# Performance work log

Hardware: AMD Instinct MI355X
Metric: run time of the kernel (lower is better)

The kernel has to match this reference:

```python
import jax, jax.numpy as jnp
import numpy as np

B, N, D, H, DK, DV = 2, 2048, 1024, 16, 64, 64
NEG = -1000000000.0
EPS = 1e-6


def setup_inputs() -> dict:
    key = jax.random.key(0)
    ks = jax.random.split(key, 8)
    s = 0.02
    return {
        "q": jax.random.normal(ks[0], (B, N, D), jnp.float32),
        "k": jax.random.normal(ks[1], (B, N, D), jnp.float32),
        "v": jax.random.normal(ks[2], (B, N, D), jnp.float32),
        "attn_mask": jnp.ones((B, N, N), jnp.int32),
        "Wq": jax.random.normal(ks[3], (D, H * DK), jnp.float32) * s,
        "Wk": jax.random.normal(ks[4], (D, H * DK), jnp.float32) * s,
        "Wv": jax.random.normal(ks[5], (D, H * DV), jnp.float32) * s,
        "Wo": jax.random.normal(ks[6], (H * DV, D), jnp.float32) * s,
        "gamma": jnp.ones((D,), jnp.float32),
        "beta": jnp.zeros((D,), jnp.float32),
    }


def reference(q, k, v, attn_mask, Wq, Wk, Wv, Wo, gamma, beta):
    b, n, _ = q.shape
    residual = q
    # project and split heads: (b, h, n, dk)
    qh = (q @ Wq).reshape(b, n, H, DK).transpose(0, 2, 1, 3)
    kh = (k @ Wk).reshape(b, n, H, DK).transpose(0, 2, 1, 3)
    vh = (v @ Wv).reshape(b, n, H, DV).transpose(0, 2, 1, 3)
    temperature = DK ** 0.5
    scores = jnp.einsum('bhnd,bhmd->bhnm', qh / temperature, kh)
    # external mask (masked where mask == 0), broadcast over heads
    scores = jnp.where(attn_mask[:, None, :, :] == 0, NEG, scores)
    # built-in causal mask (strictly upper triangle)
    causal = jnp.triu(jnp.ones((n, n), dtype=bool), k=1)
    scores = jnp.where(causal, NEG, scores)
    attn = jax.nn.softmax(scores, axis=-1)
    out = jnp.einsum('bhnm,bhmd->bnhd', attn, vh).reshape(b, n, H * DV)
    out = out @ Wo + residual
    # LayerNorm(eps=1e-6)
    mean = out.mean(-1, keepdims=True)
    var = ((out - mean) ** 2).mean(-1, keepdims=True)
    out = (out - mean) / jnp.sqrt(var + EPS) * gamma + beta
    return out, attn
```

## Files before the change

### kernel.cpp

```cpp
#include <hip/hip_runtime.h>
#include <hip/hip_bf16.h>
#include <stdint.h>

#define B_ 2
#define N_ 2048
#define D_ 1024
#define H_ 16
#define MM 4096
#define NN 1024
#define KK 1024

typedef __bf16 bf16;
typedef __bf16 bf16x8 __attribute__((ext_vector_type(8)));
typedef float f32x4 __attribute__((ext_vector_type(4)));

struct __align__(8) bf4 { bf16 v[4]; };

#define LDS_STRIDE 144

__global__ void k_wtt(const float* __restrict__ W, bf16* __restrict__ Wt) {
    __shared__ float t[32][33];
    int bx = blockIdx.x * 32, by = blockIdx.y * 32;
    int tx = threadIdx.x, ty = threadIdx.y;
#pragma unroll
    for (int j = 0; j < 32; j += 8)
        t[ty + j][tx] = W[(size_t)(by + ty + j) * 1024 + bx + tx];
    __syncthreads();
#pragma unroll
    for (int j = 0; j < 32; j += 8)
        Wt[(size_t)(bx + ty + j) * 1024 + by + tx] = (bf16)t[tx][ty + j];
}

__global__ __launch_bounds__(256) void k_bits(const int* __restrict__ mask,
                                              uint32_t* __restrict__ bits) {
    size_t flat = (size_t)blockIdx.x * 256 + threadIdx.x;
    int col = (int)(flat & (N_ - 1));
    int row = (int)((flat >> 11) & (N_ - 1));
    bool ok = (mask[flat] != 0) && (col <= row);
    unsigned long long bal = __ballot(ok);
    if ((threadIdx.x & 63) == 0)
        *(unsigned long long*)(bits + (flat >> 5)) = bal;
}

template <int MODE, bool AF32>
__global__ __launch_bounds__(256) void k_gemm(const void* __restrict__ Av,
                                              const bf16* __restrict__ Bt,
                                              bf16* __restrict__ Cb,
                                              float* __restrict__ Cf,
                                              const float* __restrict__ resid,
                                              float scale) {
    __shared__ __align__(16) char AsB[64 * LDS_STRIDE];
    __shared__ __align__(16) char BsB[128 * LDS_STRIDE];
    const int tid = threadIdx.x, lane = tid & 63, w = tid >> 6;
    const int g = lane >> 4, li = lane & 15;
    const int bm0 = blockIdx.x * 64, bn0 = blockIdx.y * 128;
    const int srow = tid >> 3, sc = tid & 7;
    const bf16* Ab = (const bf16*)Av;
    const float* Af = (const float*)Av;

    f32x4 zz = {0.f, 0.f, 0.f, 0.f};
    f32x4 acc[4][2];
#pragma unroll
    for (int mf = 0; mf < 4; ++mf)
#pragma unroll
        for (int nf = 0; nf < 2; ++nf) acc[mf][nf] = zz;

    f32x4 pa0[2], pa1[2];
    bf16x8 pab[2];
    bf16x8 pb[4];

    auto issueA = [&](int k0) {
        if constexpr (AF32) {
#pragma unroll
            for (int i = 0; i < 2; ++i) {
                const float* s = Af + (size_t)(bm0 + srow + 32 * i) * KK + k0 + sc * 8;
                pa0[i] = *(const f32x4*)s;
                pa1[i] = *(const f32x4*)(s + 4);
            }
        } else {
#pragma unroll
            for (int i = 0; i < 2; ++i)
                pab[i] = *(const bf16x8*)(Ab + (size_t)(bm0 + srow + 32 * i) * KK + k0 + sc * 8);
        }
    };
    auto issueB = [&](int k0) {
#pragma unroll
        for (int i = 0; i < 4; ++i)
            pb[i] = *(const bf16x8*)(Bt + (size_t)(bn0 + srow + 32 * i) * KK + k0 + sc * 8);
    };
    auto writeS = [&]() {
#pragma unroll
        for (int i = 0; i < 2; ++i) {
            bf16x8 t;
            if constexpr (AF32) {
#pragma unroll
                for (int j = 0; j < 4; ++j) {
                    t[j] = (bf16)pa0[i][j];
                    t[4 + j] = (bf16)pa1[i][j];
                }
            } else {
                t = pab[i];
            }
            *(bf16x8*)(AsB + (srow + 32 * i) * LDS_STRIDE + sc * 16) = t;
        }
#pragma unroll
        for (int i = 0; i < 4; ++i)
            *(bf16x8*)(BsB + (srow + 32 * i) * LDS_STRIDE + sc * 16) = pb[i];
    };

    issueA(0);
    issueB(0);
    for (int k0 = 0; k0 < KK; k0 += 64) {
        __syncthreads();
        writeS();
        int kn = (k0 + 64 < KK) ? k0 + 64 : k0;
        issueA(kn);
        issueB(kn);
        __syncthreads();
#pragma unroll
        for (int kk = 0; kk < 2; ++kk) {
            const int kb = kk * 64 + (g << 4);
            bf16x8 bfr[2];
#pragma unroll
            for (int nf = 0; nf < 2; ++nf) {
                int rn = w * 32 + nf * 16 + li;
                bfr[nf] = *(const bf16x8*)(BsB + rn * LDS_STRIDE + kb);
            }
#pragma unroll
            for (int mf = 0; mf < 4; ++mf) {
                int rm = mf * 16 + li;
                bf16x8 afr = *(const bf16x8*)(AsB + rm * LDS_STRIDE + kb);
                acc[mf][0] = __builtin_amdgcn_mfma_f32_16x16x32_bf16(
                    afr, bfr[0], acc[mf][0], 0, 0, 0);
                acc[mf][1] = __builtin_amdgcn_mfma_f32_16x16x32_bf16(
                    afr, bfr[1], acc[mf][1], 0, 0, 0);
            }
        }
    }
#pragma unroll
    for (int mf = 0; mf < 4; ++mf)
#pragma unroll
        for (int nf = 0; nf < 2; ++nf) {
            int n = bn0 + w * 32 + nf * 16 + li;
            int m0 = bm0 + mf * 16 + (g << 2);
            if (MODE == 0) {
#pragma unroll
                for (int r = 0; r < 4; ++r)
                    Cb[(size_t)(m0 + r) * NN + n] = (bf16)(acc[mf][nf][r] * scale);
            } else if (MODE == 1) {
                int bq = m0 >> 11, tok = m0 & (N_ - 1);
                int hh = n >> 6, dv = n & 63;
                bf4 val;
#pragma unroll
                for (int r = 0; r < 4; ++r) val.v[r] = (bf16)(acc[mf][nf][r] * scale);
                *(bf4*)(Cb + ((size_t)((bq * H_ + hh) * 64 + dv)) * N_ + tok) = val;
            } else {
#pragma unroll
                for (int r = 0; r < 4; ++r) {
                    size_t ix = (size_t)(m0 + r) * NN + n;
                    Cf[ix] = acc[mf][nf][r] + resid[ix];
                }
            }
        }
}

__global__ __launch_bounds__(256) void k_attn(const bf16* __restrict__ Qh,
                                              const bf16* __restrict__ Kh,
                                              const bf16* __restrict__ Vt,
                                              const uint32_t* __restrict__ bits,
                                              float* __restrict__ attnp,
                                              bf16* __restrict__ Ob) {
    __shared__ __align__(16) char Qs[64 * LDS_STRIDE];
    __shared__ __align__(16) char Ks[64 * LDS_STRIDE];
    __shared__ __align__(16) char Vs[64 * LDS_STRIDE];
    __shared__ __align__(16) char Ps[64 * LDS_STRIDE];
    const int tid = threadIdx.x, lane = tid & 63, w = tid >> 6;
    const int g = lane >> 4, li = lane & 15;
    const int p = blockIdx.x, h = blockIdx.y, b = blockIdx.z;
    const int srow = tid >> 3, sc = tid & 7;
    const int myrow = w * 16 + li;

    const size_t kbase = ((size_t)b * N_) * D_ + h * 64;
    const size_t vbase = ((size_t)(b * H_ + h) * 64) * N_;
    f32x4 zz = {0.f, 0.f, 0.f, 0.f};

    for (int half = 0; half < 2; ++half) {
        const int qt = half ? (31 - p) : p;
        const int i0 = qt << 6;
        const size_t abase = (((size_t)b * H_ + h) * N_ + i0) * (size_t)N_;

        __syncthreads();
        {
            const char* qsrc = (const char*)Qh +
                (kbase + (size_t)(i0 + srow) * D_ + sc * 8) * 2;
            bf16x8 t0 = *(const bf16x8*)qsrc;
            bf16x8 t1 = *(const bf16x8*)(qsrc + (size_t)32 * D_ * 2);
            *(bf16x8*)(Qs + srow * LDS_STRIDE + sc * 16) = t0;
            *(bf16x8*)(Qs + (srow + 32) * LDS_STRIDE + sc * 16) = t1;
        }
        const uint32_t* mrow = bits + (((size_t)b * N_ + i0 + myrow) << 6);

        float m = -1e30f, l = 0.f;
        bf16x8 ka, kb2;
        {
            const char* ks = (const char*)Kh + (kbase + (size_t)srow * D_ + sc * 8) * 2;
            ka = *(const bf16x8*)ks;
            kb2 = *(const bf16x8*)(ks + (size_t)32 * D_ * 2);
        }
        for (int jt = 0; jt <= qt; ++jt) {
            __syncthreads();
            *(bf16x8*)(Ks + srow * LDS_STRIDE + sc * 16) = ka;
            *(bf16x8*)(Ks + (srow + 32) * LDS_STRIDE + sc * 16) = kb2;
            {
                int jn = (jt < qt) ? jt + 1 : qt;
                const char* ks = (const char*)Kh +
                    (kbase + (size_t)(jn * 64 + srow) * D_ + sc * 8) * 2;
                ka = *(const bf16x8*)ks;
                kb2 = *(const bf16x8*)(ks + (size_t)32 * D_ * 2);
            }
            uint2 mw = *(const uint2*)(mrow + (jt << 1));
            __syncthreads();

            f32x4 s[4];
#pragma unroll
            for (int mf = 0; mf < 4; ++mf) s[mf] = zz;
#pragma unroll
            for (int kk = 0; kk < 2; ++kk) {
                const int kb = kk * 64 + (g << 4);
                bf16x8 qf = *(const bf16x8*)(Qs + myrow * LDS_STRIDE + kb);
#pragma unroll
                for (int mf = 0; mf < 4; ++mf) {
                    bf16x8 kf = *(const bf16x8*)(Ks + (mf * 16 + li) * LDS_STRIDE + kb);
                    s[mf] = __builtin_amdgcn_mfma_f32_16x16x32_bf16(kf, qf, s[mf], 0, 0, 0);
                }
            }
            float tmax = m;
#pragma unroll
            for (int mf = 0; mf < 4; ++mf) {
                uint32_t wsel = (mf < 2) ? mw.x : mw.y;
#pragma unroll
                for (int r = 0; r < 4; ++r) {
                    int sh = (mf & 1) * 16 + g * 4 + r;
                    float xv = ((wsel >> sh) & 1) ? s[mf][r] : -1e9f;
                    s[mf][r] = xv;
                    tmax = fmaxf(tmax, xv);
                }
            }
            tmax = fmaxf(tmax, __shfl_xor(tmax, 16));
            tmax = fmaxf(tmax, __shfl_xor(tmax, 32));
            float ps = 0.f;
#pragma unroll
            for (int mf = 0; mf < 4; ++mf)
#pragma unroll
                for (int r = 0; r < 4; ++r) ps += __expf(s[mf][r] - tmax);
            ps += __shfl_xor(ps, 16);
            ps += __shfl_xor(ps, 32);
            l = l * __expf(m - tmax) + ps;
            m = tmax;
        }
        const float linv = 1.0f / l;

        f32x4 oacc[4];
#pragma unroll
        for (int nf = 0; nf < 4; ++nf) oacc[nf] = zz;

        bf16x8 va, vb2;
        {
            const char* ks = (const char*)Kh + (kbase + (size_t)srow * D_ + sc * 8) * 2;
            ka = *(const bf16x8*)ks;
            kb2 = *(const bf16x8*)(ks + (size_t)32 * D_ * 2);
            const char* vs = (const char*)Vt + (vbase + (size_t)srow * N_ + sc * 8) * 2;
            va = *(const bf16x8*)vs;
            vb2 = *(const bf16x8*)(vs + (size_t)32 * N_ * 2);
        }
        for (int jt = 0; jt <= qt; ++jt) {
            __syncthreads();
            *(bf16x8*)(Ks + srow * LDS_STRIDE + sc * 16) = ka;
            *(bf16x8*)(Ks + (srow + 32) * LDS_STRIDE + sc * 16) = kb2;
            *(bf16x8*)(Vs + srow * LDS_STRIDE + sc * 16) = va;
            *(bf16x8*)(Vs + (srow + 32) * LDS_STRIDE + sc * 16) = vb2;
            {
                int jn = (jt < qt) ? jt + 1 : qt;
                const char* ks = (const char*)Kh +
                    (kbase + (size_t)(jn * 64 + srow) * D_ + sc * 8) * 2;
                ka = *(const bf16x8*)ks;
                kb2 = *(const bf16x8*)(ks + (size_t)32 * D_ * 2);
                const char* vs = (const char*)Vt +
                    (vbase + (size_t)srow * N_ + jn * 64 + sc * 8) * 2;
                va = *(const bf16x8*)vs;
                vb2 = *(const bf16x8*)(vs + (size_t)32 * N_ * 2);
            }
            uint2 mw = *(const uint2*)(mrow + (jt << 1));
            __syncthreads();

            f32x4 s[4];
#pragma unroll
            for (int mf = 0; mf < 4; ++mf) s[mf] = zz;
#pragma unroll
            for (int kk = 0; kk < 2; ++kk) {
                const int kb = kk * 64 + (g << 4);
                bf16x8 qf = *(const bf16x8*)(Qs + myrow * LDS_STRIDE + kb);
#pragma unroll
                for (int mf = 0; mf < 4; ++mf) {
                    bf16x8 kf = *(const bf16x8*)(Ks + (mf * 16 + li) * LDS_STRIDE + kb);
                    s[mf] = __builtin_amdgcn_mfma_f32_16x16x32_bf16(kf, qf, s[mf], 0, 0, 0);
                }
            }
#pragma unroll
            for (int mf = 0; mf < 4; ++mf) {
                uint32_t wsel = (mf < 2) ? mw.x : mw.y;
#pragma unroll
                for (int r = 0; r < 4; ++r) {
                    int sh = (mf & 1) * 16 + g * 4 + r;
                    float xv = ((wsel >> sh) & 1) ? s[mf][r] : -1e9f;
                    s[mf][r] = __expf(xv - m) * linv;
                }
                *(f32x4*)(attnp + abase + (size_t)myrow * N_ + (jt << 6) + mf * 16 + g * 4) = s[mf];
                bf4 pk;
#pragma unroll
                for (int r = 0; r < 4; ++r) pk.v[r] = (bf16)s[mf][r];
                *(bf4*)(Ps + myrow * LDS_STRIDE + (mf * 16 + g * 4) * 2) = pk;
            }
#pragma unroll
            for (int kk = 0; kk < 2; ++kk) {
                const int kb = kk * 64 + (g << 4);
                bf16x8 pf = *(const bf16x8*)(Ps + myrow * LDS_STRIDE + kb);
#pragma unroll
                for (int nf = 0; nf < 4; ++nf) {
                    bf16x8 vf = *(const bf16x8*)(Vs + (nf * 16 + li) * LDS_STRIDE + kb);
                    oacc[nf] = __builtin_amdgcn_mfma_f32_16x16x32_bf16(pf, vf, oacc[nf], 0, 0, 0);
                }
            }
        }
#pragma unroll
        for (int nf = 0; nf < 4; ++nf)
#pragma unroll
            for (int r = 0; r < 4; ++r) {
                int gi = i0 + w * 16 + g * 4 + r;
                Ob[((size_t)(b * N_ + gi)) * D_ + h * 64 + nf * 16 + li] = (bf16)oacc[nf][r];
            }
        int zc0 = i0 + 64;
        if (zc0 < N_) {
            int r = tid >> 2, tc = tid & 3;
            f32x4 z = zz;
            for (int c = zc0 + tc * 4; c < N_; c += 16)
                *(f32x4*)(attnp + abase + (size_t)r * N_ + c) = z;
        }
    }
}

__global__ __launch_bounds__(256) void k_ln(float* __restrict__ out,
                                            const float* __restrict__ gamma,
                                            const float* __restrict__ beta) {
    const int row = blockIdx.x, t = threadIdx.x, lane = t & 63, w = t >> 6;
    float* p = out + (size_t)row * D_;
    f32x4 x = *(const f32x4*)(p + t * 4);
    float s = x[0] + x[1] + x[2] + x[3];
    float s2 = x[0] * x[0] + x[1] * x[1] + x[2] * x[2] + x[3] * x[3];
#pragma unroll
    for (int o = 1; o < 64; o <<= 1) {
        s += __shfl_xor(s, o);
        s2 += __shfl_xor(s2, o);
    }
    __shared__ float r1[4], r2[4];
    if (lane == 0) { r1[w] = s; r2[w] = s2; }
    __syncthreads();
    s = r1[0] + r1[1] + r1[2] + r1[3];
    s2 = r2[0] + r2[1] + r2[2] + r2[3];
    float mean = s * (1.f / D_);
    float var = s2 * (1.f / D_) - mean * mean;
    float rstd = rsqrtf(var + 1e-6f);
    f32x4 gv = *(const f32x4*)(gamma + t * 4);
    f32x4 bv = *(const f32x4*)(beta + t * 4);
    f32x4 y;
#pragma unroll
    for (int c = 0; c < 4; ++c) y[c] = (x[c] - mean) * rstd * gv[c] + bv[c];
    *(f32x4*)(p + t * 4) = y;
}

extern "C" void kernel_launch(void* const* d_in, const int* in_sizes, int n_in,
                              void* d_out, int out_size, void* d_ws,
                              size_t ws_size, hipStream_t stream) {
    (void)in_sizes; (void)n_in; (void)out_size; (void)ws_size;
    const float* q = (const float*)d_in[0];
    const float* k = (const float*)d_in[1];
    const float* v = (const float*)d_in[2];
    const int* msk = (const int*)d_in[3];
    const float* Wq = (const float*)d_in[4];
    const float* Wk = (const float*)d_in[5];
    const float* Wv = (const float*)d_in[6];
    const float* Wo = (const float*)d_in[7];
    const float* gamma = (const float*)d_in[8];
    const float* beta = (const float*)d_in[9];

    float* outp = (float*)d_out;
    float* attnp = outp + (size_t)B_ * N_ * D_;

    const size_t U = (size_t)B_ * N_ * D_;
    const size_t W1 = (size_t)D_ * D_;
    bf16* ws = (bf16*)d_ws;
    bf16* WqT = ws;  ws += W1;
    bf16* WkT = ws;  ws += W1;
    bf16* WvT = ws;  ws += W1;
    bf16* WoT = ws;  ws += W1;
    bf16* Qh = ws;   ws += U;
    bf16* Kh = ws;   ws += U;
    bf16* Vt = ws;   ws += U;
    bf16* Ob = ws;   ws += U;
    uint32_t* bits = (uint32_t*)ws;

    dim3 tb(32, 8);
    k_wtt<<<dim3(32, 32), tb, 0, stream>>>(Wq, WqT);
    k_wtt<<<dim3(32, 32), tb, 0, stream>>>(Wk, WkT);
    k_wtt<<<dim3(32, 32), tb, 0, stream>>>(Wv, WvT);
    k_wtt<<<dim3(32, 32), tb, 0, stream>>>(Wo, WoT);
    k_bits<<<(size_t)B_ * N_ * N_ / 256, 256, 0, stream>>>(msk, bits);

    dim3 gg(MM / 64, NN / 128);
    k_gemm<0, true><<<gg, 256, 0, stream>>>(q, WqT, Qh, nullptr, nullptr, 0.125f);
    k_gemm<0, true><<<gg, 256, 0, stream>>>(k, WkT, Kh, nullptr, nullptr, 1.0f);
    k_gemm<1, true><<<gg, 256, 0, stream>>>(v, WvT, Vt, nullptr, nullptr, 1.0f);

    k_attn<<<dim3(16, H_, B_), 256, 0, stream>>>(Qh, Kh, Vt, bits, attnp, Ob);

    k_gemm<2, false><<<gg, 256, 0, stream>>>(Ob, WoT, nullptr, outp, q, 1.0f);

    k_ln<<<B_ * N_, 256, 0, stream>>>(outp, gamma, beta);
}
```

Before: 285.9 us.

## Restructure GEMMs with direct-to-LDS loads, batch QKV projections, double-buffer attention

A new kernel converts q/k/v to bf16 up front, and the three projection GEMMs are merged into one launch. The GEMM core now uses 128x128 tiles with global_load_lds direct copies and a swizzled block order. The attention kernel double-buffers its K/V tiles in LDS so the next tile loads while the current one is computed. Attention-probability stores become nontemporal. These target GEMM memory traffic, launch overhead and attention load latency, at the cost of an extra conversion pass and more LDS use.

New measurement: 300.2 us. +5.0%, slower.

```diff
diff --git a/kernel.cpp b/kernel.cpp
--- a/kernel.cpp
+++ b/kernel.cpp
@@ -17,6 +17,29 @@
 struct __align__(8) bf4 { bf16 v[4]; };
 
 #define LDS_STRIDE 144
+
+#define GLDS(gp, lp)                                                     \
+    __builtin_amdgcn_global_load_lds(                                    \
+        (const __attribute__((address_space(1))) void*)(gp),             \
+        (__attribute__((address_space(3))) void*)(lp), 16, 0, 0)
+
+__global__ __launch_bounds__(256) void k_cvt3(const float* __restrict__ q,
+                                              const float* __restrict__ k,
+                                              const float* __restrict__ v,
+                                              bf16* __restrict__ qb,
+                                              bf16* __restrict__ kb,
+                                              bf16* __restrict__ vb) {
+    const int z = blockIdx.y;
+    const float* s = z == 0 ? q : z == 1 ? k : v;
+    bf16* d = z == 0 ? qb : z == 1 ? kb : vb;
+    size_t i = ((size_t)blockIdx.x * 256 + threadIdx.x) * 8;
+    f32x4 a = *(const f32x4*)(s + i);
+    f32x4 b = *(const f32x4*)(s + i + 4);
+    bf16x8 o;
+#pragma unroll
+    for (int j = 0; j < 4; ++j) { o[j] = (bf16)a[j]; o[4 + j] = (bf16)b[j]; }
+    *(bf16x8*)(d + i) = o;
+}
 
 __global__ void k_wtt(const float* __restrict__ W, bf16* __restrict__ Wt) {
     __shared__ float t[32][33];
@@ -42,124 +65,144 @@
         *(unsigned long long*)(bits + (flat >> 5)) = bal;
 }
 
-template <int MODE, bool AF32>
-__global__ __launch_bounds__(256) void k_gemm(const void* __restrict__ Av,
-                                              const bf16* __restrict__ Bt,
-                                              bf16* __restrict__ Cb,
-                                              float* __restrict__ Cf,
-                                              const float* __restrict__ resid,
-                                              float scale) {
-    __shared__ __align__(16) char AsB[64 * LDS_STRIDE];
-    __shared__ __align__(16) char BsB[128 * LDS_STRIDE];
-    const int tid = threadIdx.x, lane = tid & 63, w = tid >> 6;
+__device__ __forceinline__ void mm_core(const bf16* __restrict__ A,
+                                        const bf16* __restrict__ Bt,
+                                        int bm0, int bn0,
+                                        bf16* As, bf16* Bs,
+                                        f32x4 (&acc)[4][4]) {
+    const int tid = threadIdx.x, w = tid >> 6, lane = tid & 63;
     const int g = lane >> 4, li = lane & 15;
-    const int bm0 = blockIdx.x * 64, bn0 = blockIdx.y * 128;
-    const int srow = tid >> 3, sc = tid & 7;
-    const bf16* Ab = (const bf16*)Av;
-    const float* Af = (const float*)Av;
+    const int wr = w >> 1, wc = w & 1;
+    const int row = tid >> 3, cc = tid & 7;
 
     f32x4 zz = {0.f, 0.f, 0.f, 0.f};
-    f32x4 acc[4][2];
 #pragma unroll
     for (int mf = 0; mf < 4; ++mf)
 #pragma unroll
-        for (int nf = 0; nf < 2; ++nf) acc[mf][nf] = zz;
-
-    f32x4 pa0[2], pa1[2];
-    bf16x8 pab[2];
-    bf16x8 pb[4];
-
-    auto issueA = [&](int k0) {
-        if constexpr (AF32) {
-#pragma unroll
-            for (int i = 0; i < 2; ++i) {
-                const float* s = Af + (size_t)(bm0 + srow + 32 * i) * KK + k0 + sc * 8;
-                pa0[i] = *(const f32x4*)s;
-                pa1[i] = *(const f32x4*)(s + 4);
-            }
-        } else {
-#pragma unroll
-            for (int i = 0; i < 2; ++i)
-                pab[i] = *(const bf16x8*)(Ab + (size_t)(bm0 + srow + 32 * i) * KK + k0 + sc * 8);
+        for (int nf = 0; nf < 4; ++nf) acc[mf][nf] = zz;
+
+    auto stage = [&](int k0) {
+#pragma unroll
+        for (int c = 0; c < 4; ++c) {
+            int ch = c * 256 + tid;
+            int r = ch >> 3, cl = ch & 7;
+            GLDS(A + (size_t)(bm0 + r) * KK + k0 + cl * 8,
+                 As + ((size_t)c * 256 + w * 64) * 8);
+        }
+#pragma unroll
+        for (int c = 0; c < 4; ++c) {
+            int ch = c * 256 + tid;
+            int r = ch >> 3, cl = ch & 7;
+            GLDS(Bt + (size_t)(bn0 + r) * KK + k0 + cl * 8,
+                 Bs + ((size_t)c * 256 + w * 64) * 8);
         }
     };
-    auto issueB = [&](int k0) {
-#pragma unroll
-        for (int i = 0; i < 4; ++i)
-            pb[i] = *(const bf16x8*)(Bt + (size_t)(bn0 + srow + 32 * i) * KK + k0 + sc * 8);
-    };
-    auto writeS = [&]() {
-#pragma unroll
-        for (int i = 0; i < 2; ++i) {
-            bf16x8 t;
-            if constexpr (AF32) {
-#pragma unroll
-                for (int j = 0; j < 4; ++j) {
-                    t[j] = (bf16)pa0[i][j];
-                    t[4 + j] = (bf16)pa1[i][j];
-                }
-            } else {
-                t = pab[i];
-            }
-            *(bf16x8*)(AsB + (srow + 32 * i) * LDS_STRIDE + sc * 16) = t;
-        }
-#pragma unroll
-        for (int i = 0; i < 4; ++i)
-            *(bf16x8*)(BsB + (srow + 32 * i) * LDS_STRIDE + sc * 16) = pb[i];
-    };
-
-    issueA(0);
-    issueB(0);
-    for (int k0 = 0; k0 < KK; k0 += 64) {
+    (void)row; (void)cc;
+
+    stage(0);
+    for (int s = 0; s < KK / 64; ++s) {
         __syncthreads();
-        writeS();
-        int kn = (k0 + 64 < KK) ? k0 + 64 : k0;
-        issueA(kn);
-        issueB(kn);
+#pragma unroll
+        for (int kk = 0; kk < 2; ++kk) {
+            bf16x8 af[4], bfr[4];
+#pragma unroll
+            for (int i = 0; i < 4; ++i) {
+                af[i] = *(const bf16x8*)(As + (wr * 64 + i * 16 + li) * 64 + kk * 32 + g * 8);
+                bfr[i] = *(const bf16x8*)(Bs + (wc * 64 + i * 16 + li) * 64 + kk * 32 + g * 8);
+            }
+#pragma unroll
+            for (int mf = 0; mf < 4; ++mf)
+#pragma unroll
+                for (int nf = 0; nf < 4; ++nf)
+                    acc[mf][nf] = __builtin_amdgcn_mfma_f32_16x16x32_bf16(
+                        af[mf], bfr[nf], acc[mf][nf], 0, 0, 0);
+        }
         __syncthreads();
-#pragma unroll
-        for (int kk = 0; kk < 2; ++kk) {
-            const int kb = kk * 64 + (g << 4);
-            bf16x8 bfr[2];
-#pragma unroll
-            for (int nf = 0; nf < 2; ++nf) {
-                int rn = w * 32 + nf * 16 + li;
-                bfr[nf] = *(const bf16x8*)(BsB + rn * LDS_STRIDE + kb);
-            }
-#pragma unroll
-            for (int mf = 0; mf < 4; ++mf) {
-                int rm = mf * 16 + li;
-                bf16x8 afr = *(const bf16x8*)(AsB + rm * LDS_STRIDE + kb);
-                acc[mf][0] = __builtin_amdgcn_mfma_f32_16x16x32_bf16(
-                    afr, bfr[0], acc[mf][0], 0, 0, 0);
-                acc[mf][1] = __builtin_amdgcn_mfma_f32_16x16x32_bf16(
-                    afr, bfr[1], acc[mf][1], 0, 0, 0);
-            }
-        }
+        if (s + 1 < KK / 64) stage((s + 1) * 64);
     }
-#pragma unroll
-    for (int mf = 0; mf < 4; ++mf)
-#pragma unroll
-        for (int nf = 0; nf < 2; ++nf) {
-            int n = bn0 + w * 32 + nf * 16 + li;
-            int m0 = bm0 + mf * 16 + (g << 2);
-            if (MODE == 0) {
+}
+
+__global__ __launch_bounds__(256) void k_proj(const bf16* __restrict__ qb,
+                                              const bf16* __restrict__ kb,
+                                              const bf16* __restrict__ vb,
+                                              const bf16* __restrict__ WqT,
+                                              const bf16* __restrict__ WkT,
+                                              const bf16* __restrict__ WvT,
+                                              bf16* __restrict__ Qh,
+                                              bf16* __restrict__ Kh,
+                                              bf16* __restrict__ Vt) {
+    __shared__ __align__(16) bf16 As[128 * 64];
+    __shared__ __align__(16) bf16 Bs[128 * 64];
+    const int z = blockIdx.y;
+    const bf16* A = z == 0 ? qb : z == 1 ? kb : vb;
+    const bf16* Bt = z == 0 ? WqT : z == 1 ? WkT : WvT;
+    int bid = blockIdx.x;
+    int swz = (bid & 7) * 32 + (bid >> 3);
+    int bm0 = (swz >> 3) * 128, bn0 = (swz & 7) * 128;
+
+    f32x4 acc[4][4];
+    mm_core(A, Bt, bm0, bn0, As, Bs, acc);
+
+    const int tid = threadIdx.x, w = tid >> 6, lane = tid & 63;
+    const int g = lane >> 4, li = lane & 15;
+    const int wr = w >> 1, wc = w & 1;
+    const float scale = (z == 0) ? 0.125f : 1.0f;
+
+    if (z < 2) {
+        bf16* C = (z == 0) ? Qh : Kh;
+#pragma unroll
+        for (int mf = 0; mf < 4; ++mf)
+#pragma unroll
+            for (int nf = 0; nf < 4; ++nf) {
+                int m0 = bm0 + wr * 64 + mf * 16 + g * 4;
+                int n = bn0 + wc * 64 + nf * 16 + li;
 #pragma unroll
                 for (int r = 0; r < 4; ++r)
-                    Cb[(size_t)(m0 + r) * NN + n] = (bf16)(acc[mf][nf][r] * scale);
-            } else if (MODE == 1) {
+                    C[(size_t)(m0 + r) * NN + n] = (bf16)(acc[mf][nf][r] * scale);
+            }
+    } else {
+#pragma unroll
+        for (int mf = 0; mf < 4; ++mf)
+#pragma unroll
+            for (int nf = 0; nf < 4; ++nf) {
+                int m0 = bm0 + wr * 64 + mf * 16 + g * 4;
+                int n = bn0 + wc * 64 + nf * 16 + li;
                 int bq = m0 >> 11, tok = m0 & (N_ - 1);
                 int hh = n >> 6, dv = n & 63;
                 bf4 val;
 #pragma unroll
-                for (int r = 0; r < 4; ++r) val.v[r] = (bf16)(acc[mf][nf][r] * scale);
-                *(bf4*)(Cb + ((size_t)((bq * H_ + hh) * 64 + dv)) * N_ + tok) = val;
-            } else {
-#pragma unroll
-                for (int r = 0; r < 4; ++r) {
-                    size_t ix = (size_t)(m0 + r) * NN + n;
-                    Cf[ix] = acc[mf][nf][r] + resid[ix];
-                }
+                for (int r = 0; r < 4; ++r) val.v[r] = (bf16)acc[mf][nf][r];
+                *(bf4*)(Vt + ((size_t)((bq * H_ + hh) * 64 + dv)) * N_ + tok) = val;
+            }
+    }
+}
+
+__global__ __launch_bounds__(256) void k_out(const bf16* __restrict__ Ob,
+                                             const bf16* __restrict__ WoT,
+                                             float* __restrict__ outp,
+                                             const float* __restrict__ resid) {
+    __shared__ __align__(16) bf16 As[128 * 64];
+    __shared__ __align__(16) bf16 Bs[128 * 64];
+    int bid = blockIdx.x;
+    int swz = (bid & 7) * 32 + (bid >> 3);
+    int bm0 = (swz >> 3) * 128, bn0 = (swz & 7) * 128;
+
+    f32x4 acc[4][4];
+    mm_core(Ob, WoT, bm0, bn0, As, Bs, acc);
+
+    const int tid = threadIdx.x, w = tid >> 6, lane = tid & 63;
+    const int g = lane >> 4, li = lane & 15;
+    const int wr = w >> 1, wc = w & 1;
+#pragma unroll
+    for (int mf = 0; mf < 4; ++mf)
+#pragma unroll
+        for (int nf = 0; nf < 4; ++nf) {
+            int m0 = bm0 + wr * 64 + mf * 16 + g * 4;
+            int n = bn0 + wc * 64 + nf * 16 + li;
+#pragma unroll
+            for (int r = 0; r < 4; ++r) {
+                size_t ix = (size_t)(m0 + r) * NN + n;
+                outp[ix] = acc[mf][nf][r] + resid[ix];
             }
         }
 }
@@ -171,8 +214,8 @@
                                               float* __restrict__ attnp,
                                               bf16* __restrict__ Ob) {
     __shared__ __align__(16) char Qs[64 * LDS_STRIDE];
-    __shared__ __align__(16) char Ks[64 * LDS_STRIDE];
-    __shared__ __align__(16) char Vs[64 * LDS_STRIDE];
+    __shared__ __align__(16) char Ks[2][64 * LDS_STRIDE];
+    __shared__ __align__(16) char Vs[2][64 * LDS_STRIDE];
     __shared__ __align__(16) char Ps[64 * LDS_STRIDE];
     const int tid = threadIdx.x, lane = tid & 63, w = tid >> 6;
     const int g = lane >> 4, li = lane & 15;
@@ -183,6 +226,28 @@
     const size_t kbase = ((size_t)b * N_) * D_ + h * 64;
     const size_t vbase = ((size_t)(b * H_ + h) * 64) * N_;
     f32x4 zz = {0.f, 0.f, 0.f, 0.f};
+
+    bf16x8 ka, kb2, va, vb2;
+    auto loadK = [&](int jt) {
+        const char* ks = (const char*)Kh +
+            (kbase + (size_t)(jt * 64 + srow) * D_ + sc * 8) * 2;
+        ka = *(const bf16x8*)ks;
+        kb2 = *(const bf16x8*)(ks + (size_t)32 * D_ * 2);
+    };
+    auto loadV = [&](int jt) {
+        const char* vs = (const char*)Vt +
+            (vbase + (size_t)srow * N_ + jt * 64 + sc * 8) * 2;
+        va = *(const bf16x8*)vs;
+        vb2 = *(const bf16x8*)(vs + (size_t)32 * N_ * 2);
+    };
+    auto writeK = [&](int bi) {
+        *(bf16x8*)(Ks[bi] + srow * LDS_STRIDE + sc * 16) = ka;
+        *(bf16x8*)(Ks[bi] + (srow + 32) * LDS_STRIDE + sc * 16) = kb2;
+    };
+    auto writeV = [&](int bi) {
+        *(bf16x8*)(Vs[bi] + srow * LDS_STRIDE + sc * 16) = va;
+        *(bf16x8*)(Vs[bi] + (srow + 32) * LDS_STRIDE + sc * 16) = vb2;
+    };
 
     for (int half = 0; half < 2; ++half) {
         const int qt = half ? (31 - p) : p;
@@ -201,25 +266,13 @@
         const uint32_t* mrow = bits + (((size_t)b * N_ + i0 + myrow) << 6);
 
         float m = -1e30f, l = 0.f;
-        bf16x8 ka, kb2;
-        {
-            const char* ks = (const char*)Kh + (kbase + (size_t)srow * D_ + sc * 8) * 2;
-            ka = *(const bf16x8*)ks;
-            kb2 = *(const bf16x8*)(ks + (size_t)32 * D_ * 2);
-        }
+        loadK(0);
+        writeK(0);
         for (int jt = 0; jt <= qt; ++jt) {
-            __syncthreads();
-            *(bf16x8*)(Ks + srow * LDS_STRIDE + sc * 16) = ka;
-            *(bf16x8*)(Ks + (srow + 32) * LDS_STRIDE + sc * 16) = kb2;
-            {
-                int jn = (jt < qt) ? jt + 1 : qt;
-                const char* ks = (const char*)Kh +
-                    (kbase + (size_t)(jn * 64 + srow) * D_ + sc * 8) * 2;
-                ka = *(const bf16x8*)ks;
-                kb2 = *(const bf16x8*)(ks + (size_t)32 * D_ * 2);
-            }
+            if (jt < qt) loadK(jt + 1);
             uint2 mw = *(const uint2*)(mrow + (jt << 1));
             __syncthreads();
+            const char* Kb = Ks[jt & 1];
 
             f32x4 s[4];
 #pragma unroll
@@ -230,10 +283,12 @@
                 bf16x8 qf = *(const bf16x8*)(Qs + myrow * LDS_STRIDE + kb);
 #pragma unroll
                 for (int mf = 0; mf < 4; ++mf) {
-                    bf16x8 kf = *(const bf16x8*)(Ks + (mf * 16 + li) * LDS_STRIDE + kb);
+                    bf16x8 kf = *(const bf16x8*)(Kb + (mf * 16 + li) * LDS_STRIDE + kb);
                     s[mf] = __builtin_amdgcn_mfma_f32_16x16x32_bf16(kf, qf, s[mf], 0, 0, 0);
                 }
             }
+            if (jt < qt) writeK((jt + 1) & 1);
+
             float tmax = m;
 #pragma unroll
             for (int mf = 0; mf < 4; ++mf) {
@@ -264,34 +319,17 @@
 #pragma unroll
         for (int nf = 0; nf < 4; ++nf) oacc[nf] = zz;
 
-        bf16x8 va, vb2;
-        {
-            const char* ks = (const char*)Kh + (kbase + (size_t)srow * D_ + sc * 8) * 2;
-            ka = *(const bf16x8*)ks;
-            kb2 = *(const bf16x8*)(ks + (size_t)32 * D_ * 2);
-            const char* vs = (const char*)Vt + (vbase + (size_t)srow * N_ + sc * 8) * 2;
-            va = *(const bf16x8*)vs;
-            vb2 = *(const bf16x8*)(vs + (size_t)32 * N_ * 2);
-        }
+        __syncthreads();
+        loadK(0);
+        loadV(0);
+        writeK(0);
+        writeV(0);
         for (int jt = 0; jt <= qt; ++jt) {
-            __syncthreads();
-            *(bf16x8*)(Ks + srow * LDS_STRIDE + sc * 16) = ka;
-            *(bf16x8*)(Ks + (srow + 32) * LDS_STRIDE + sc * 16) = kb2;
-            *(bf16x8*)(Vs + srow * LDS_STRIDE + sc * 16) = va;
-            *(bf16x8*)(Vs + (srow + 32) * LDS_STRIDE + sc * 16) = vb2;
-            {
-                int jn = (jt < qt) ? jt + 1 : qt;
-                const char* ks = (const char*)Kh +
-                    (kbase + (size_t)(jn * 64 + srow) * D_ + sc * 8) * 2;
-                ka = *(const bf16x8*)ks;
-                kb2 = *(const bf16x8*)(ks + (size_t)32 * D_ * 2);
-                const char* vs = (const char*)Vt +
-                    (vbase + (size_t)srow * N_ + jn * 64 + sc * 8) * 2;
-                va = *(const bf16x8*)vs;
-                vb2 = *(const bf16x8*)(vs + (size_t)32 * N_ * 2);
-            }
+            if (jt < qt) { loadK(jt + 1); loadV(jt + 1); }
             uint2 mw = *(const uint2*)(mrow + (jt << 1));
             __syncthreads();
+            const char* Kb = Ks[jt & 1];
+            const char* Vb = Vs[jt & 1];
 
             f32x4 s[4];
 #pragma unroll
@@ -302,10 +340,12 @@
                 bf16x8 qf = *(const bf16x8*)(Qs + myrow * LDS_STRIDE + kb);
 #pragma unroll
                 for (int mf = 0; mf < 4; ++mf) {
-                    bf16x8 kf = *(const bf16x8*)(Ks + (mf * 16 + li) * LDS_STRIDE + kb);
+                    bf16x8 kf = *(const bf16x8*)(Kb + (mf * 16 + li) * LDS_STRIDE + kb);
                     s[mf] = __builtin_amdgcn_mfma_f32_16x16x32_bf16(kf, qf, s[mf], 0, 0, 0);
                 }
             }
+            if (jt < qt) { writeK((jt + 1) & 1); writeV((jt + 1) & 1); }
+
 #pragma unroll
             for (int mf = 0; mf < 4; ++mf) {
                 uint32_t wsel = (mf < 2) ? mw.x : mw.y;
@@ -315,7 +355,8 @@
                     float xv = ((wsel >> sh) & 1) ? s[mf][r] : -1e9f;
                     s[mf][r] = __expf(xv - m) * linv;
                 }
-                *(f32x4*)(attnp + abase + (size_t)myrow * N_ + (jt << 6) + mf * 16 + g * 4) = s[mf];
+                __builtin_nontemporal_store(s[mf],
+                    (f32x4*)(attnp + abase + (size_t)myrow * N_ + (jt << 6) + mf * 16 + g * 4));
                 bf4 pk;
 #pragma unroll
                 for (int r = 0; r < 4; ++r) pk.v[r] = (bf16)s[mf][r];
@@ -327,7 +368,7 @@
                 bf16x8 pf = *(const bf16x8*)(Ps + myrow * LDS_STRIDE + kb);
 #pragma unroll
                 for (int nf = 0; nf < 4; ++nf) {
-                    bf16x8 vf = *(const bf16x8*)(Vs + (nf * 16 + li) * LDS_STRIDE + kb);
+                    bf16x8 vf = *(const bf16x8*)(Vb + (nf * 16 + li) * LDS_STRIDE + kb);
                     oacc[nf] = __builtin_amdgcn_mfma_f32_16x16x32_bf16(pf, vf, oacc[nf], 0, 0, 0);
                 }
             }
@@ -344,7 +385,7 @@
             int r = tid >> 2, tc = tid & 3;
             f32x4 z = zz;
             for (int c = zc0 + tc * 4; c < N_; c += 16)
-                *(f32x4*)(attnp + abase + (size_t)r * N_ + c) = z;
+                __builtin_nontemporal_store(z, (f32x4*)(attnp + abase + (size_t)r * N_ + c));
         }
     }
 }
@@ -399,6 +440,9 @@
     const size_t U = (size_t)B_ * N_ * D_;
     const size_t W1 = (size_t)D_ * D_;
     bf16* ws = (bf16*)d_ws;
+    bf16* qb = ws;   ws += U;
+    bf16* kb = ws;   ws += U;
+    bf16* vb = ws;   ws += U;
     bf16* WqT = ws;  ws += W1;
     bf16* WkT = ws;  ws += W1;
     bf16* WvT = ws;  ws += W1;
@@ -409,6 +453,7 @@
     bf16* Ob = ws;   ws += U;
     uint32_t* bits = (uint32_t*)ws;
 
+    k_cvt3<<<dim3(U / 8 / 256, 3), 256, 0, stream>>>(q, k, v, qb, kb, vb);
     dim3 tb(32, 8);
     k_wtt<<<dim3(32, 32), tb, 0, stream>>>(Wq, WqT);
     k_wtt<<<dim3(32, 32), tb, 0, stream>>>(Wk, WkT);
@@ -416,14 +461,11 @@
     k_wtt<<<dim3(32, 32), tb, 0, stream>>>(Wo, WoT);
     k_bits<<<(size_t)B_ * N_ * N_ / 256, 256, 0, stream>>>(msk, bits);
 
-    dim3 gg(MM / 64, NN / 128);
-    k_gemm<0, true><<<gg, 256, 0, stream>>>(q, WqT, Qh, nullptr, nullptr, 0.125f);
-    k_gemm<0, true><<<gg, 256, 0, stream>>>(k, WkT, Kh, nullptr, nullptr, 1.0f);
-    k_gemm<1, true><<<gg, 256, 0, stream>>>(v, WvT, Vt, nullptr, nullptr, 1.0f);
+    k_proj<<<dim3(256, 3), 256, 0, stream>>>(qb, kb, vb, WqT, WkT, WvT, Qh, Kh, Vt);
 
     k_attn<<<dim3(16, H_, B_), 256, 0, stream>>>(Qh, Kh, Vt, bits, attnp, Ob);
 
-    k_gemm<2, false><<<gg, 256, 0, stream>>>(Ob, WoT, nullptr, outp, q, 1.0f);
+    k_out<<<256, 256, 0, stream>>>(Ob, WoT, outp, q);
 
     k_ln<<<B_ * N_, 256, 0, stream>>>(outp, gamma, beta);
 }
```
